# Optimization experiments

Measured on AMD Instinct MI355X. Metric: run time of the kernel, lower is better.

## Reference

```python
import jax, jax.numpy as jnp
from jax import lax
import numpy as np

EPS = 1e-5


def _convlstm_layer(x, w, b):
    # x: [B, T, Cin, H, W]; w: [4*hid, Cin+hid, 3, 3]; b: [4*hid]
    B, T, Cin, H, W = x.shape
    hid = w.shape[0] // 4

    def step(carry, xt):
        h, c = carry
        z = lax.conv_general_dilated(
            jnp.concatenate([xt, h], axis=1), w, (1, 1), 'SAME',
            dimension_numbers=('NCHW', 'OIHW', 'NCHW')) + b[None, :, None, None]
        i, f, o, g = jnp.split(z, 4, axis=1)
        c_next = jax.nn.sigmoid(f) * c + jax.nn.sigmoid(i) * jnp.tanh(g)
        h_next = jax.nn.sigmoid(o) * jnp.tanh(c_next)
        return (h_next, c_next), h_next

    h0 = jnp.zeros((B, hid, H, W), x.dtype)
    (_, _), hs = lax.scan(step, (h0, h0), jnp.moveaxis(x, 1, 0))
    return jnp.moveaxis(hs, 0, 1)  # [B, T, hid, H, W]


def _bn_relu_pool(h, gamma, beta):
    # h: [B, T, C, H, W] -> BatchNorm3d (training stats) + ReLU + MaxPool3d(1,2,2)
    x = jnp.moveaxis(h, 1, 2)  # [B, C, T, H, W]
    mu = x.mean(axis=(0, 2, 3, 4), keepdims=True)
    var = x.var(axis=(0, 2, 3, 4), keepdims=True)
    x = (x - mu) * lax.rsqrt(var + EPS)
    x = x * gamma[None, :, None, None, None] + beta[None, :, None, None, None]
    x = jax.nn.relu(x)
    B, C, T, H, W = x.shape
    x = x.reshape(B, C, T, H // 2, 2, W // 2, 2).max(axis=(4, 6))
    return jnp.moveaxis(x, 2, 1)  # [B, T, C, H//2, W//2]


def setup_inputs() -> dict:
    key = jax.random.key(0)
    ks = jax.random.split(key, 16)
    B, T, H, W = 8, 40, 64, 64
    dims = [(1, 16), (16, 32), (32, 64), (64, 64)]
    inp = {'x': jax.random.normal(ks[0], (B, T, 1, H, W), jnp.float32)}
    for l, (cin, hid) in enumerate(dims, 1):
        fan = (cin + hid) * 9
        inp[f'w{l}'] = jax.random.normal(ks[l], (4 * hid, cin + hid, 3, 3), jnp.float32) / np.sqrt(fan)
        inp[f'b{l}'] = jnp.zeros((4 * hid,), jnp.float32)
        inp[f'gamma{l}'] = jnp.ones((hid,), jnp.float32)
        inp[f'beta{l}'] = jnp.zeros((hid,), jnp.float32)
    feat_dim = 64 * (H // 16) * (W // 16)  # 1024
    inp['fc1_w'] = jax.random.normal(ks[10], (128, feat_dim), jnp.float32) / np.sqrt(feat_dim)
    inp['fc1_b'] = jnp.zeros((128,), jnp.float32)
    inp['fc2_w'] = jax.random.normal(ks[11], (2, 128), jnp.float32) / np.sqrt(128.0)
    inp['fc2_b'] = jnp.zeros((2,), jnp.float32)
    return inp


def reference(x, w1, b1, gamma1, beta1, w2, b2, gamma2, beta2,
              w3, b3, gamma3, beta3, w4, b4, gamma4, beta4,
              fc1_w, fc1_b, fc2_w, fc2_b):
    h = _convlstm_layer(x, w1, b1)
    h = _bn_relu_pool(h, gamma1, beta1)
    h = _convlstm_layer(h, w2, b2)
    h = _bn_relu_pool(h, gamma2, beta2)
    h = _convlstm_layer(h, w3, b3)
    h = _bn_relu_pool(h, gamma3, beta3)
    h = _convlstm_layer(h, w4, b4)
    h = _bn_relu_pool(h, gamma4, beta4)  # [B, T, 64, 4, 4]
    B, T = h.shape[0], h.shape[1]
    feat = h.reshape(B, T, -1)  # [B, T, 1024]
    f1 = jax.nn.relu(jnp.einsum('btd,kd->btk', feat, fc1_w) + fc1_b)
    y = jnp.einsum('btk,ok->bto', f1, fc2_w) + fc2_b  # [B, T, 2]
    return y
```

## Files before the change

### kernel.cpp

```cpp
#include <hip/hip_runtime.h>
#include <math.h>

#define DEV __device__ __forceinline__

DEV float sigmoid_(float x) { return 1.0f / (1.0f + __expf(-x)); }
DEV float tanh_(float x) {
    float e = __expf(2.0f * x);
    return 1.0f - 2.0f / (e + 1.0f);
}

template<int TPB, int OCL, int RPT>
__global__ __launch_bounds__(TPB) void zx_k(
    const float* __restrict__ xin, const float* __restrict__ w,
    const float* __restrict__ bias, float* __restrict__ zx,
    int t0, int TcAct, int TcMax, int B, int T, int Cin, int Ctot,
    int hid, int H, int W, int nOcg, int BPP)
{
    const int HW = H * W;
    int blk   = blockIdx.x;
    int chunk = blk % BPP;
    int ocg   = (blk / BPP) % nOcg;
    int tc    = (blk / (BPP * nOcg)) % TcAct;
    int b     = blk / (BPP * nOcg * TcAct);
    int oc0   = ocg * OCL;

    int p    = threadIdx.x;
    int col  = p % W;
    int rowg = p / W;
    int rpc  = (TPB / W) * RPT;
    int y0   = chunk * rpc + rowg * RPT;

    int   off[RPT + 2][3];
    float msk[RPT + 2][3];
    #pragma unroll
    for (int dy = 0; dy < RPT + 2; ++dy) {
        int yy = y0 + dy - 1;
        #pragma unroll
        for (int dx = 0; dx < 3; ++dx) {
            int xx = col + dx - 1;
            bool ok = (yy >= 0 && yy < H && xx >= 0 && xx < W);
            off[dy][dx] = ok ? yy * W + xx : 0;
            msk[dy][dx] = ok ? 1.0f : 0.0f;
        }
    }

    float z[RPT][OCL][4];
    #pragma unroll
    for (int r = 0; r < RPT; ++r)
        #pragma unroll
        for (int j = 0; j < OCL; ++j)
            #pragma unroll
            for (int g = 0; g < 4; ++g)
                z[r][j][g] = bias[g * hid + oc0 + j];

    const float* xsl = xin + ((size_t)(b * T + t0 + tc) * Cin) * HW;
    for (int ic = 0; ic < Cin; ++ic) {
        const float* src = xsl + (size_t)ic * HW;
        float v[RPT + 2][3];
        #pragma unroll
        for (int dy = 0; dy < RPT + 2; ++dy)
            #pragma unroll
            for (int dx = 0; dx < 3; ++dx)
                v[dy][dx] = src[off[dy][dx]] * msk[dy][dx];

        #pragma unroll
        for (int j = 0; j < OCL; ++j)
            #pragma unroll
            for (int g = 0; g < 4; ++g) {
                const float* wp = w + ((size_t)(g * hid + oc0 + j) * Ctot + ic) * 9;
                #pragma unroll
                for (int k = 0; k < 9; ++k) {
                    float wv = wp[k];
                    #pragma unroll
                    for (int r = 0; r < RPT; ++r)
                        z[r][j][g] = fmaf(v[r + k / 3][k % 3], wv, z[r][j][g]);
                }
            }
    }

    size_t base = ((size_t)(b * TcMax + tc) * 4 * hid) * HW;
    #pragma unroll
    for (int r = 0; r < RPT; ++r) {
        size_t rb = base + (size_t)(y0 + r) * W + col;
        #pragma unroll
        for (int j = 0; j < OCL; ++j)
            #pragma unroll
            for (int g = 0; g < 4; ++g)
                zx[rb + (size_t)(g * hid + oc0 + j) * HW] = z[r][j][g];
    }
}

template<int TPB, int OCL, int CIN, int TCB>
__global__ __launch_bounds__(TPB) void zx_lds(
    const float* __restrict__ xin, const float* __restrict__ w,
    const float* __restrict__ bias, float* __restrict__ zx,
    int t0, int TcAct, int TcMax, int B, int T, int Ctot, int hid,
    int H, int W, int nOcg, int BPP, int nTcb)
{
    const int HW  = H * W;
    const int PIX = TPB / TCB;
    alignas(16) __shared__ float wlds[OCL * CIN * 36];

    int blk   = blockIdx.x;
    int chunk = blk % BPP;
    int ocg   = (blk / BPP) % nOcg;
    int tcb   = (blk / (BPP * nOcg)) % nTcb;
    int b     = blk / (BPP * nOcg * nTcb);
    int oc0   = ocg * OCL;

    for (int i = threadIdx.x; i < OCL * CIN * 36; i += TPB) {
        int g   = i & 3;
        int k   = (i >> 2) % 9;
        int ic  = (i / 36) % CIN;
        int ocl = i / (36 * CIN);
        wlds[i] = w[((size_t)(g * hid + oc0 + ocl) * Ctot + ic) * 9 + k];
    }
    __syncthreads();

    int tcl = threadIdx.x / PIX;
    int p   = threadIdx.x % PIX;
    int tc  = tcb * TCB + tcl;
    if (tc >= TcAct) return;

    int px  = chunk * PIX + p;
    int col = px % W;
    int y0  = px / W;

    int   off[3][3];
    float msk[3][3];
    #pragma unroll
    for (int dy = 0; dy < 3; ++dy) {
        int yy = y0 + dy - 1;
        #pragma unroll
        for (int dx = 0; dx < 3; ++dx) {
            int xx = col + dx - 1;
            bool ok = (yy >= 0 && yy < H && xx >= 0 && xx < W);
            off[dy][dx] = ok ? yy * W + xx : 0;
            msk[dy][dx] = ok ? 1.0f : 0.0f;
        }
    }

    float z[OCL][4];
    #pragma unroll
    for (int j = 0; j < OCL; ++j)
        #pragma unroll
        for (int g = 0; g < 4; ++g)
            z[j][g] = bias[g * hid + oc0 + j];

    const float* xsl = xin + ((size_t)(b * T + t0 + tc) * CIN) * HW;
    for (int ic = 0; ic < CIN; ++ic) {
        const float* src = xsl + (size_t)ic * HW;
        float v[3][3];
        #pragma unroll
        for (int dy = 0; dy < 3; ++dy)
            #pragma unroll
            for (int dx = 0; dx < 3; ++dx)
                v[dy][dx] = src[off[dy][dx]] * msk[dy][dx];

        #pragma unroll
        for (int j = 0; j < OCL; ++j) {
            #pragma unroll
            for (int k = 0; k < 9; ++k) {
                const float4 wv = *(const float4*)&wlds[(((j * CIN + ic) * 9) + k) * 4];
                float vv = v[k / 3][k % 3];
                z[j][0] = fmaf(vv, wv.x, z[j][0]);
                z[j][1] = fmaf(vv, wv.y, z[j][1]);
                z[j][2] = fmaf(vv, wv.z, z[j][2]);
                z[j][3] = fmaf(vv, wv.w, z[j][3]);
            }
        }
    }

    size_t base = ((size_t)(b * TcMax + tc) * 4 * hid) * HW + (size_t)y0 * W + col;
    #pragma unroll
    for (int j = 0; j < OCL; ++j)
        #pragma unroll
        for (int g = 0; g < 4; ++g)
            zx[base + (size_t)(g * hid + oc0 + j) * HW] = z[j][g];
}

template<int TPB, int OCB, int RPT>
__global__ __launch_bounds__(TPB) void step_h(
    const float* __restrict__ zx,
    const float* __restrict__ w,
    float* __restrict__ hbuf,
    float* __restrict__ cbuf,
    int t, int tc, int TcMax, int B, int T, int Cin, int hid, int H, int W,
    int nOcg, int BPP)
{
    extern __shared__ float wlds[];
    const int HW = H * W;
    const int Ctot = Cin + hid;

    int blk   = blockIdx.x;
    int chunk = blk % BPP;
    int ocg   = (blk / BPP) % nOcg;
    int b     = blk / (BPP * nOcg);
    int oc0   = ocg * OCB;

    if (t > 0) {
        int tot = OCB * hid * 36;
        for (int i = threadIdx.x; i < tot; i += TPB) {
            int ocb = i / (hid * 36);
            int rem = i % (hid * 36);
            int ic  = rem / 36;
            int gk  = rem % 36;
            int g = gk / 9, k = gk % 9;
            wlds[i] = w[((size_t)(g * hid + oc0 + ocb) * Ctot + Cin + ic) * 9 + k];
        }
        __syncthreads();
    }

    const int TPO = TPB / OCB;
    int ocb  = threadIdx.x / TPO;
    int p    = threadIdx.x % TPO;
    int oc   = oc0 + ocb;
    int col  = p % W;
    int rowg = p / W;
    const int chunkRows = (TPO / W) * RPT;
    int y0 = chunk * chunkRows + rowg * RPT;

    float z[RPT][4];
    size_t zb0 = ((size_t)(b * TcMax + tc) * 4 * hid) * HW;
    #pragma unroll
    for (int r = 0; r < RPT; ++r) {
        size_t zb = zb0 + (size_t)(y0 + r) * W + col;
        #pragma unroll
        for (int g = 0; g < 4; ++g)
            z[r][g] = zx[zb + (size_t)(g * hid + oc) * HW];
    }

    if (t > 0) {
        const float* hsl = hbuf + ((size_t)(b * T + (t - 1)) * hid) * HW;
        for (int ic = 0; ic < hid; ++ic) {
            const float* src = hsl + (size_t)ic * HW;
            float v[RPT + 2][3];
            #pragma unroll
            for (int dy = 0; dy < RPT + 2; ++dy) {
                int yy = y0 + dy - 1;
                #pragma unroll
                for (int dx = 0; dx < 3; ++dx) {
                    int xx = col + dx - 1;
                    v[dy][dx] = (yy >= 0 && yy < H && xx >= 0 && xx < W)
                                ? src[yy * W + xx] : 0.0f;
                }
            }
            float wv[36];
            const float* wp = &wlds[(ocb * hid + ic) * 36];
            #pragma unroll
            for (int j = 0; j < 36; ++j) wv[j] = wp[j];
            #pragma unroll
            for (int r = 0; r < RPT; ++r)
                #pragma unroll
                for (int g = 0; g < 4; ++g)
                    #pragma unroll
                    for (int k = 0; k < 9; ++k)
                        z[r][g] = fmaf(v[r + k / 3][k % 3], wv[g * 9 + k], z[r][g]);
        }
    }

    #pragma unroll
    for (int r = 0; r < RPT; ++r) {
        int y = y0 + r;
        size_t ci = ((size_t)b * hid + oc) * HW + (size_t)y * W + col;
        float cprev = (t == 0) ? 0.0f : cbuf[ci];
        float ig = sigmoid_(z[r][0]);
        float fg = sigmoid_(z[r][1]);
        float og = sigmoid_(z[r][2]);
        float gg = tanh_(z[r][3]);
        float cn = fg * cprev + ig * gg;
        cbuf[ci] = cn;
        hbuf[((size_t)(b * T + t) * hid + oc) * HW + (size_t)y * W + col]
            = og * tanh_(cn);
    }
}

__global__ void bn_stats(const float* __restrict__ hbuf, float* __restrict__ stats,
                         int BT, int C, int HW)
{
    int c = blockIdx.x;
    float s = 0.0f, s2 = 0.0f;
    for (int bt = blockIdx.y; bt < BT; bt += gridDim.y) {
        const float* p = hbuf + ((size_t)bt * C + c) * HW;
        for (int i = threadIdx.x; i < HW; i += blockDim.x) {
            float v = p[i];
            s += v;
            s2 += v * v;
        }
    }
    __shared__ float ssum[256];
    __shared__ float ssq[256];
    int tid = threadIdx.x;
    ssum[tid] = s; ssq[tid] = s2;
    __syncthreads();
    for (int off = 128; off > 0; off >>= 1) {
        if (tid < off) { ssum[tid] += ssum[tid + off]; ssq[tid] += ssq[tid + off]; }
        __syncthreads();
    }
    if (tid == 0) {
        atomicAdd(&stats[2 * c + 0], ssum[0]);
        atomicAdd(&stats[2 * c + 1], ssq[0]);
    }
}

__global__ void bn_relu_pool(const float* __restrict__ hbuf,
                             const float* __restrict__ stats,
                             const float* __restrict__ gamma,
                             const float* __restrict__ beta,
                             float* __restrict__ out,
                             int BT, int C, int H, int W, float invN)
{
    int Ho = H / 2, Wo = W / 2;
    int idx = blockIdx.x * blockDim.x + threadIdx.x;
    int total = BT * C * Ho * Wo;
    if (idx >= total) return;
    int xo = idx % Wo;
    int yo = (idx / Wo) % Ho;
    int c  = (idx / (Wo * Ho)) % C;
    int bt = idx / (C * Ho * Wo);

    float mean = stats[2 * c + 0] * invN;
    float var  = stats[2 * c + 1] * invN - mean * mean;
    float sc = gamma[c] * rsqrtf(var + 1e-5f);
    float sh = beta[c] - mean * sc;

    const float* p = hbuf + ((size_t)bt * C + c) * (H * W) + (2 * yo) * W + 2 * xo;
    float a0 = fmaxf(fmaf(p[0],     sc, sh), 0.0f);
    float a1 = fmaxf(fmaf(p[1],     sc, sh), 0.0f);
    float a2 = fmaxf(fmaf(p[W],     sc, sh), 0.0f);
    float a3 = fmaxf(fmaf(p[W + 1], sc, sh), 0.0f);
    out[idx] = fmaxf(fmaxf(a0, a1), fmaxf(a2, a3));
}

__global__ __launch_bounds__(128) void fc_head(const float* __restrict__ feat,
                                               const float* __restrict__ fc1w,
                                               const float* __restrict__ fc1b,
                                               const float* __restrict__ fc2w,
                                               const float* __restrict__ fc2b,
                                               float* __restrict__ out)
{
    __shared__ float sf[1024];
    __shared__ float y1[128];
    int bt = blockIdx.x;
    const float* f = feat + (size_t)bt * 1024;
    for (int i = threadIdx.x; i < 1024; i += 128) sf[i] = f[i];
    __syncthreads();
    int k = threadIdx.x;
    float acc = fc1b[k];
    const float* wk = fc1w + (size_t)k * 1024;
    for (int d = 0; d < 1024; ++d) acc = fmaf(sf[d], wk[d], acc);
    y1[k] = fmaxf(acc, 0.0f);
    __syncthreads();
    if (k < 2) {
        float a = fc2b[k];
        const float* w2 = fc2w + k * 128;
        for (int j = 0; j < 128; ++j) a = fmaf(y1[j], w2[j], a);
        out[(size_t)bt * 2 + k] = a;
    }
}

static void launch_zx(int l, const float* in, const float* w, const float* bias,
                      float* zbuf, int t0, int TcAct, int TcMax, int B, int T,
                      int Cin, int hid, int H, int W, hipStream_t s)
{
    int Ctot = Cin + hid;
    switch (l) {
        case 0: {
            zx_k<256,4,2><<<B*TcAct*4*8, 256, 0, s>>>(
                in,w,bias,zbuf,t0,TcAct,TcMax,B,T,Cin,Ctot,hid,H,W,4,8); } break;
        case 1: {
            zx_lds<256,4,16,1><<<B*TcAct*8*4, 256, 0, s>>>(
                in,w,bias,zbuf,t0,TcAct,TcMax,B,T,Ctot,hid,H,W,8,4,TcAct); } break;
        case 2: {
            zx_lds<256,4,32,1><<<B*TcAct*16, 256, 0, s>>>(
                in,w,bias,zbuf,t0,TcAct,TcMax,B,T,Ctot,hid,H,W,16,1,TcAct); } break;
        case 3: {
            int nTcb = (TcAct + 3) / 4;
            zx_lds<256,4,64,4><<<B*nTcb*16, 256, 0, s>>>(
                in,w,bias,zbuf,t0,TcAct,TcMax,B,T,Ctot,hid,H,W,16,1,nTcb); } break;
    }
}

static void launch_step(int l, const float* zbuf, const float* w,
                        float* hbuf, float* cbuf, int t, int tc, int TcMax,
                        int B, int T, int Cin, int hid, int H, int W, hipStream_t s)
{
    const int HW = H * W;
    const int OCB = (l == 3) ? 4 : 1;
    const int RPT = (l < 2) ? 2 : 1;
    const int TPO = 256 / OCB;
    const int CH  = TPO * RPT;
    const int BPP = HW / CH;
    const int nOcg = hid / OCB;
    const int blocks = B * nOcg * BPP;
    const size_t lds = (size_t)OCB * hid * 36 * sizeof(float);

    switch (l) {
        case 0: step_h<256,1,2><<<blocks,256,lds,s>>>(zbuf,w,hbuf,cbuf,t,tc,TcMax,B,T,Cin,hid,H,W,nOcg,BPP); break;
        case 1: step_h<256,1,2><<<blocks,256,lds,s>>>(zbuf,w,hbuf,cbuf,t,tc,TcMax,B,T,Cin,hid,H,W,nOcg,BPP); break;
        case 2: step_h<256,1,1><<<blocks,256,lds,s>>>(zbuf,w,hbuf,cbuf,t,tc,TcMax,B,T,Cin,hid,H,W,nOcg,BPP); break;
        case 3: step_h<256,4,1><<<blocks,256,lds,s>>>(zbuf,w,hbuf,cbuf,t,tc,TcMax,B,T,Cin,hid,H,W,nOcg,BPP); break;
    }
}

extern "C" void kernel_launch(void* const* d_in, const int* in_sizes, int n_in,
                              void* d_out, int out_size, void* d_ws, size_t ws_size,
                              hipStream_t stream)
{
    const int B = 8, T = 40;
    const float* x = (const float*)d_in[0];

    float* hbuf  = (float*)d_ws;
    float* pbuf  = hbuf + (size_t)20971520;
    float* cbuf  = pbuf + (size_t)5242880;
    float* stats = cbuf + (size_t)524288;
    float* zbuf  = stats + 128;

    struct LCfg { int Cin, hid, H, W, Tc; };
    const LCfg L[4] = { {1, 16, 64, 64, 4}, {16, 32, 32, 32, 8},
                        {32, 64, 16, 16, 16}, {64, 64, 8, 8, 40} };

    const float* in = x;
    for (int l = 0; l < 4; ++l) {
        const float* w     = (const float*)d_in[1 + 4 * l];
        const float* bias  = (const float*)d_in[2 + 4 * l];
        const float* gamma = (const float*)d_in[3 + 4 * l];
        const float* beta  = (const float*)d_in[4 + 4 * l];
        const int Cin = L[l].Cin, hid = L[l].hid, H = L[l].H, W = L[l].W;
        const int HW = H * W;
        const int TcMax = L[l].Tc;

        for (int t0 = 0; t0 < T; t0 += TcMax) {
            int TcAct = (T - t0 < TcMax) ? (T - t0) : TcMax;
            launch_zx(l, in, w, bias, zbuf, t0, TcAct, TcMax, B, T, Cin, hid, H, W, stream);
            for (int t = t0; t < t0 + TcAct; ++t)
                launch_step(l, zbuf, w, hbuf, cbuf, t, t - t0, TcMax,
                            B, T, Cin, hid, H, W, stream);
        }

        hipMemsetAsync(stats, 0, 2 * hid * sizeof(float), stream);
        bn_stats<<<dim3(hid, 80), 256, 0, stream>>>(hbuf, stats, B * T, hid, HW);

        int ptotal = B * T * hid * (H / 2) * (W / 2);
        float invN = 1.0f / ((float)(B * T) * (float)HW);
        bn_relu_pool<<<(ptotal + 255) / 256, 256, 0, stream>>>(
            hbuf, stats, gamma, beta, pbuf, B * T, hid, H, W, invN);
        in = pbuf;
    }

    const float* fc1w = (const float*)d_in[17];
    const float* fc1b = (const float*)d_in[18];
    const float* fc2w = (const float*)d_in[19];
    const float* fc2b = (const float*)d_in[20];
    fc_head<<<B * T, 128, 0, stream>>>(pbuf, fc1w, fc1b, fc2w, fc2b, (float*)d_out);
}
```

Measured before the change: 5.475 ms.

## Stage hidden-state halo tiles in LDS for recurrent step kernel

```diff
diff --git a/kernel.cpp b/kernel.cpp
--- a/kernel.cpp
+++ b/kernel.cpp
@@ -179,100 +179,94 @@
             zx[base + (size_t)(g * hid + oc0 + j) * HW] = z[j][g];
 }
 
-template<int TPB, int OCB, int RPT>
-__global__ __launch_bounds__(TPB) void step_h(
+template<int TPB, int OCB, int ROWS, int HID, int H, int W>
+__global__ __launch_bounds__(TPB) void step_t(
     const float* __restrict__ zx,
     const float* __restrict__ w,
     float* __restrict__ hbuf,
     float* __restrict__ cbuf,
-    int t, int tc, int TcMax, int B, int T, int Cin, int hid, int H, int W,
-    int nOcg, int BPP)
-{
-    extern __shared__ float wlds[];
+    int t, int tc, int TcMax, int B, int T, int Cin, int nOcg, int BPP)
+{
     const int HW = H * W;
-    const int Ctot = Cin + hid;
+    const int Ctot = Cin + HID;
+    const int TH = ROWS + 2, TW = W + 2;
+    __shared__ float tile[HID][TH][TW];
+    alignas(16) __shared__ float wlds[OCB][HID][9][4];
 
     int blk   = blockIdx.x;
     int chunk = blk % BPP;
     int ocg   = (blk / BPP) % nOcg;
     int b     = blk / (BPP * nOcg);
     int oc0   = ocg * OCB;
+    int y0    = chunk * ROWS;
 
     if (t > 0) {
-        int tot = OCB * hid * 36;
-        for (int i = threadIdx.x; i < tot; i += TPB) {
-            int ocb = i / (hid * 36);
-            int rem = i % (hid * 36);
-            int ic  = rem / 36;
-            int gk  = rem % 36;
-            int g = gk / 9, k = gk % 9;
-            wlds[i] = w[((size_t)(g * hid + oc0 + ocb) * Ctot + Cin + ic) * 9 + k];
+        for (int i = threadIdx.x; i < OCB * HID * 36; i += TPB) {
+            int g   = i & 3;
+            int k   = (i >> 2) % 9;
+            int ic  = (i / 36) % HID;
+            int ocb = i / (36 * HID);
+            ((float*)wlds)[i] =
+                w[((size_t)(g * HID + oc0 + ocb) * Ctot + Cin + ic) * 9 + k];
+        }
+        const float* hsl = hbuf + ((size_t)(b * T + (t - 1)) * HID) * HW;
+        for (int i = threadIdx.x; i < HID * TH * TW; i += TPB) {
+            int rx = i % TW;
+            int ry = (i / TW) % TH;
+            int ic = i / (TW * TH);
+            int gy = y0 + ry - 1;
+            int gx = rx - 1;
+            float val = 0.0f;
+            if (gy >= 0 && gy < H && gx >= 0 && gx < W)
+                val = hsl[(size_t)ic * HW + gy * W + gx];
+            ((float*)tile)[i] = val;
         }
         __syncthreads();
     }
 
     const int TPO = TPB / OCB;
-    int ocb  = threadIdx.x / TPO;
-    int p    = threadIdx.x % TPO;
-    int oc   = oc0 + ocb;
-    int col  = p % W;
-    int rowg = p / W;
-    const int chunkRows = (TPO / W) * RPT;
-    int y0 = chunk * chunkRows + rowg * RPT;
-
-    float z[RPT][4];
-    size_t zb0 = ((size_t)(b * TcMax + tc) * 4 * hid) * HW;
-    #pragma unroll
-    for (int r = 0; r < RPT; ++r) {
-        size_t zb = zb0 + (size_t)(y0 + r) * W + col;
-        #pragma unroll
-        for (int g = 0; g < 4; ++g)
-            z[r][g] = zx[zb + (size_t)(g * hid + oc) * HW];
-    }
+    int ocb = threadIdx.x / TPO;
+    int p   = threadIdx.x % TPO;
+    int r   = p / W;
+    int x   = p % W;
+    int oc  = oc0 + ocb;
+    int y   = y0 + r;
+
+    float z[4];
+    size_t zb = ((size_t)(b * TcMax + tc) * 4 * HID) * HW + (size_t)y * W + x;
+    #pragma unroll
+    for (int g = 0; g < 4; ++g)
+        z[g] = zx[zb + (size_t)(g * HID + oc) * HW];
 
     if (t > 0) {
-        const float* hsl = hbuf + ((size_t)(b * T + (t - 1)) * hid) * HW;
-        for (int ic = 0; ic < hid; ++ic) {
-            const float* src = hsl + (size_t)ic * HW;
-            float v[RPT + 2][3];
-            #pragma unroll
-            for (int dy = 0; dy < RPT + 2; ++dy) {
-                int yy = y0 + dy - 1;
+        for (int ic = 0; ic < HID; ++ic) {
+            float v[3][3];
+            #pragma unroll
+            for (int dy = 0; dy < 3; ++dy)
                 #pragma unroll
-                for (int dx = 0; dx < 3; ++dx) {
-                    int xx = col + dx - 1;
-                    v[dy][dx] = (yy >= 0 && yy < H && xx >= 0 && xx < W)
-                                ? src[yy * W + xx] : 0.0f;
-                }
+                for (int dx = 0; dx < 3; ++dx)
+                    v[dy][dx] = tile[ic][r + dy][x + dx];
+            #pragma unroll
+            for (int k = 0; k < 9; ++k) {
+                const float4 wv = *(const float4*)&wlds[ocb][ic][k][0];
+                float vv = v[k / 3][k % 3];
+                z[0] = fmaf(vv, wv.x, z[0]);
+                z[1] = fmaf(vv, wv.y, z[1]);
+                z[2] = fmaf(vv, wv.z, z[2]);
+                z[3] = fmaf(vv, wv.w, z[3]);
             }
-            float wv[36];
-            const float* wp = &wlds[(ocb * hid + ic) * 36];
-            #pragma unroll
-            for (int j = 0; j < 36; ++j) wv[j] = wp[j];
-            #pragma unroll
-            for (int r = 0; r < RPT; ++r)
-                #pragma unroll
-                for (int g = 0; g < 4; ++g)
-                    #pragma unroll
-                    for (int k = 0; k < 9; ++k)
-                        z[r][g] = fmaf(v[r + k / 3][k % 3], wv[g * 9 + k], z[r][g]);
-        }
-    }
-
-    #pragma unroll
-    for (int r = 0; r < RPT; ++r) {
-        int y = y0 + r;
-        size_t ci = ((size_t)b * hid + oc) * HW + (size_t)y * W + col;
-        float cprev = (t == 0) ? 0.0f : cbuf[ci];
-        float ig = sigmoid_(z[r][0]);
-        float fg = sigmoid_(z[r][1]);
-        float og = sigmoid_(z[r][2]);
-        float gg = tanh_(z[r][3]);
-        float cn = fg * cprev + ig * gg;
-        cbuf[ci] = cn;
-        hbuf[((size_t)(b * T + t) * hid + oc) * HW + (size_t)y * W + col]
-            = og * tanh_(cn);
-    }
+        }
+    }
+
+    size_t ci = ((size_t)b * HID + oc) * HW + (size_t)y * W + x;
+    float cprev = (t == 0) ? 0.0f : cbuf[ci];
+    float ig = sigmoid_(z[0]);
+    float fg = sigmoid_(z[1]);
+    float og = sigmoid_(z[2]);
+    float gg = tanh_(z[3]);
+    float cn = fg * cprev + ig * gg;
+    cbuf[ci] = cn;
+    hbuf[((size_t)(b * T + t) * HID + oc) * HW + (size_t)y * W + x] = og * tanh_(cn);
 }
 
 __global__ void bn_stats(const float* __restrict__ hbuf, float* __restrict__ stats,
@@ -385,21 +379,15 @@
                         float* hbuf, float* cbuf, int t, int tc, int TcMax,
                         int B, int T, int Cin, int hid, int H, int W, hipStream_t s)
 {
-    const int HW = H * W;
-    const int OCB = (l == 3) ? 4 : 1;
-    const int RPT = (l < 2) ? 2 : 1;
-    const int TPO = 256 / OCB;
-    const int CH  = TPO * RPT;
-    const int BPP = HW / CH;
-    const int nOcg = hid / OCB;
-    const int blocks = B * nOcg * BPP;
-    const size_t lds = (size_t)OCB * hid * 36 * sizeof(float);
-
     switch (l) {
-        case 0: step_h<256,1,2><<<blocks,256,lds,s>>>(zbuf,w,hbuf,cbuf,t,tc,TcMax,B,T,Cin,hid,H,W,nOcg,BPP); break;
-        case 1: step_h<256,1,2><<<blocks,256,lds,s>>>(zbuf,w,hbuf,cbuf,t,tc,TcMax,B,T,Cin,hid,H,W,nOcg,BPP); break;
-        case 2: step_h<256,1,1><<<blocks,256,lds,s>>>(zbuf,w,hbuf,cbuf,t,tc,TcMax,B,T,Cin,hid,H,W,nOcg,BPP); break;
-        case 3: step_h<256,4,1><<<blocks,256,lds,s>>>(zbuf,w,hbuf,cbuf,t,tc,TcMax,B,T,Cin,hid,H,W,nOcg,BPP); break;
+        case 0:
+            step_t<256,4,1,16,64,64><<<2048,256,0,s>>>(zbuf,w,hbuf,cbuf,t,tc,TcMax,B,T,Cin, 4,64); break;
+        case 1:
+            step_t<256,4,2,32,32,32><<<1024,256,0,s>>>(zbuf,w,hbuf,cbuf,t,tc,TcMax,B,T,Cin, 8,16); break;
+        case 2:
+            step_t<256,4,4,64,16,16><<< 512,256,0,s>>>(zbuf,w,hbuf,cbuf,t,tc,TcMax,B,T,Cin,16, 4); break;
+        case 3:
+            step_t<256,4,8,64, 8, 8><<< 128,256,0,s>>>(zbuf,w,hbuf,cbuf,t,tc,TcMax,B,T,Cin,16, 1); break;
     }
 }
 
```

After: 5.255 ms. 4.0% less time.
